# Performance work log

Measured on AMD Instinct MI355X. Metric: run time of the kernel, lower is better.

Reference implementation:

```python
import jax, jax.numpy as jnp
import numpy as np

M, N, P, D = 256, 512, 24, 8


def _se(X, Y):
    # base squared-exponential kernel between point sets: exp(-0.5*||x-y||^2)
    d2 = jnp.sum(X * X, -1)[:, None] + jnp.sum(Y * Y, -1)[None, :] - 2.0 * (X @ Y.T)
    return jnp.exp(-0.5 * jnp.maximum(d2, 0.0))


def _pairwise_dist(X1, A1, X2, A2):
    # vectorized version of the original double loop over metric(f1, f2)
    m, p, d = X1.shape
    n, q, _ = X2.shape
    # cross terms: C[i,j] = a_i @ K(x_i, x_j) @ a_j   (one big Gram, batched quadratic form)
    K12 = _se(X1.reshape(m * p, d), X2.reshape(n * q, d)).reshape(m, p, n, q)
    C = jnp.einsum('iu,iujv,jv->ij', A1, K12, A2)
    # self terms: s_i = a_i @ K(x_i, x_i) @ a_i (computed ONCE, not per inner iteration)
    s1 = jnp.einsum('iu,iuv,iv->i', A1, jax.vmap(_se)(X1, X1), A1)
    s2 = jnp.einsum('ju,juv,jv->j', A2, jax.vmap(_se)(X2, X2), A2)
    d2 = s1[:, None] + s2[None, :] - 2.0 * C
    # matches lax.cond(d2 <= 0, 0.0, sqrt(d2))
    return jnp.sqrt(jnp.maximum(d2, 0.0))


def _kernel(rho, X1, A1, X2, A2):
    # SquaredExponential profile applied to d / sqrt(rho)
    u = _pairwise_dist(X1, A1, X2, A2) / jnp.sqrt(rho)
    return jnp.exp(-0.5 * u * u)


def setup_inputs() -> dict:
    key = jax.random.key(0)
    k = jax.random.split(key, 5)
    return {
        'X_test': jax.random.normal(k[0], (M, P, D), jnp.float32),
        'A_test': 0.2 * jax.random.normal(k[1], (M, P), jnp.float32),
        'X_obs': jax.random.normal(k[2], (N, P, D), jnp.float32),
        'A_obs': 0.2 * jax.random.normal(k[3], (N, P), jnp.float32),
        'observed_ys': jax.random.normal(k[4], (N,), jnp.float32),
        'rho': jnp.asarray(4.0, jnp.float32),
        'g': jnp.asarray(1e-3, jnp.float32),
        'nu': jnp.asarray(1.0, jnp.float32),
        'b': jnp.asarray(0.0, jnp.float32),
    }


def reference(X_test, A_test, X_obs, A_obs, observed_ys, rho, g, nu, b):
    # predict(): Kxx, Kox, Koo then gp_posterior
    Kxx = nu * _kernel(rho, X_test, A_test, X_test, A_test)          # [M, M]
    Kox = nu * _kernel(rho, X_obs, A_obs, X_test, A_test)            # [N, M]
    Koo = nu * (_kernel(rho, X_obs, A_obs, X_obs, A_obs) + g * jnp.eye(N, dtype=X_obs.dtype))

    gain = jnp.linalg.solve(Koo, Kox).T                              # [M, N]
    mean = b + gain @ (observed_ys - b)                              # [M]
    cov = Kxx - gain @ Kox                                           # [M, M]
    Kbx = jnp.ones((1, N), Koo.dtype) @ gain.T                       # [1, M]
    # 1^T Koo^{-1} 1 == inv(Koo).sum(), computed via a solve
    Koo_inv_sum = jnp.linalg.solve(Koo, jnp.ones((N,), Koo.dtype)).sum()
    cov = cov + (1.0 - Kbx).T @ (1.0 - Kbx) / Koo_inv_sum
    # stack mean on top of cov -> [M+1, M]
    return jnp.concatenate([mean[None, :], cov], axis=0)
```

## Files before the change

### kernel.cpp

```cpp
#include <hip/hip_runtime.h>
#include <cmath>

#define M 256
#define N 512
#define P 24
#define D 8

__global__ __launch_bounds__(64) void self_kernel(const float* __restrict__ X_test,
                                                  const float* __restrict__ A_test,
                                                  const float* __restrict__ X_obs,
                                                  const float* __restrict__ A_obs,
                                                  float* __restrict__ s1,
                                                  float* __restrict__ s2,
                                                  float* __restrict__ atT,
                                                  float* __restrict__ atO,
                                                  double* __restrict__ Bc) {
    const int bid = blockIdx.x;
    const int lane = threadIdx.x;
    if (bid == M + N) {
#pragma unroll
        for (int t = 0; t < 8; ++t) Bc[(size_t)256 * 512 + 64 * t + lane] = 1.0;
        return;
    }
    const float* X; const float* A; float* s; float* at; int i;
    if (bid < M) { X = X_test; A = A_test; s = s1; at = atT; i = bid; }
    else         { X = X_obs;  A = A_obs;  s = s2; at = atO; i = bid - M; }
    const float* Xi = X + (size_t)i * P * D;
    const float* Ai = A + (size_t)i * P;
    float acc = 0.f;
#pragma unroll
    for (int t = 0; t < 9; ++t) {
        int idx = lane + 64 * t;
        int u = idx / 24;
        int v = idx - u * 24;
        const float* xu = Xi + u * D;
        const float* xv = Xi + v * D;
        float d2 = 0.f;
#pragma unroll
        for (int d = 0; d < D; ++d) { float df = xu[d] - xv[d]; d2 = fmaf(df, df, d2); }
        acc = fmaf(Ai[u] * Ai[v], __expf(-0.5f * d2), acc);
    }
#pragma unroll
    for (int off = 1; off < 64; off <<= 1) acc += __shfl_xor(acc, off, 64);
    if (lane == 0) s[i] = acc;
    if (lane < 24) {
        const float* xp = Xi + lane * D;
        float q = 0.f;
#pragma unroll
        for (int d = 0; d < D; ++d) q = fmaf(xp[d], xp[d], q);
        at[(size_t)i * P + lane] = Ai[lane] * __expf(-0.5f * q);
    }
}

__global__ __launch_bounds__(128) void gram_kernel(
    const float* __restrict__ Xt, const float* __restrict__ atT, const float* __restrict__ s1,
    const float* __restrict__ Xo, const float* __restrict__ atO, const float* __restrict__ s2,
    const float* __restrict__ rho_p, const float* __restrict__ nu_p, const float* __restrict__ g_p,
    float* __restrict__ KoxT, float* __restrict__ Kxx, double* __restrict__ Koo,
    double* __restrict__ Bc) {
    const int mode = blockIdx.z;
    const int it = blockIdx.x, jt = blockIdx.y;
    const float *X1, *AT1, *S1, *X2, *AT2, *S2;
    if (mode == 0) {
        if (jt > 2 * it + 1) return;
        X1 = Xo; AT1 = atO; S1 = s2; X2 = Xo; AT2 = atO; S2 = s2;
    } else if (mode == 1) {
        if (jt >= 32) return;
        X1 = Xo; AT1 = atO; S1 = s2; X2 = Xt; AT2 = atT; S2 = s1;
    } else {
        if (it >= 16 || jt >= 32 || jt < 2 * it) return;
        X1 = Xt; AT1 = atT; S1 = s1; X2 = Xt; AT2 = atT; S2 = s1;
    }
    const int i0 = it * 16, j0 = jt * 8;
    const int tid = threadIdx.x;
    const int il = tid >> 3, uc = tid & 7;
    const int i = i0 + il;

    __shared__ __align__(16) float X2s[8 * 192];
    __shared__ float A2s[8 * 24];
    __shared__ float S2s[8];
    {
        const float4* gx = (const float4*)(X2 + (size_t)j0 * 192);
        float4* lx = (float4*)X2s;
        for (int idx = tid; idx < 8 * 48; idx += 128) lx[idx] = gx[idx];
        for (int idx = tid; idx < 8 * 24; idx += 128) A2s[idx] = AT2[(size_t)j0 * 24 + idx];
        if (tid < 8) S2s[tid] = S2[j0 + tid];
    }
    __syncthreads();

    float x1r[3][8], at1r[3];
#pragma unroll
    for (int ss = 0; ss < 3; ++ss) {
        const float* p = X1 + ((size_t)i * P + uc * 3 + ss) * D;
#pragma unroll
        for (int d = 0; d < D; ++d) x1r[ss][d] = p[d];
        at1r[ss] = AT1[(size_t)i * P + uc * 3 + ss];
    }
    const float s1i = S1[i];
    const float rho = rho_p[0], nu = nu_p[0], g = g_p[0];

    for (int jj = 0; jj < 8; ++jj) {
        const float* xb = X2s + jj * 192;
        float e0 = 0.f, e1 = 0.f, e2 = 0.f;
#pragma unroll 4
        for (int v = 0; v < 24; ++v) {
            const float4 q0 = ((const float4*)(xb + v * 8))[0];
            const float4 q1 = ((const float4*)(xb + v * 8))[1];
            float x2r[8];
            x2r[0] = q0.x; x2r[1] = q0.y; x2r[2] = q0.z; x2r[3] = q0.w;
            x2r[4] = q1.x; x2r[5] = q1.y; x2r[6] = q1.z; x2r[7] = q1.w;
            const float w2 = A2s[jj * 24 + v];
            float d0 = 0.f, d1 = 0.f, d2 = 0.f;
#pragma unroll
            for (int dd = 0; dd < 8; ++dd) {
                d0 = fmaf(x1r[0][dd], x2r[dd], d0);
                d1 = fmaf(x1r[1][dd], x2r[dd], d1);
                d2 = fmaf(x1r[2][dd], x2r[dd], d2);
            }
            e0 = fmaf(w2, __expf(d0), e0);
            e1 = fmaf(w2, __expf(d1), e1);
            e2 = fmaf(w2, __expf(d2), e2);
        }
        float acc = at1r[0] * e0;
        acc = fmaf(at1r[1], e1, acc);
        acc = fmaf(at1r[2], e2, acc);
        acc += __shfl_xor(acc, 1, 8);
        acc += __shfl_xor(acc, 2, 8);
        acc += __shfl_xor(acc, 4, 8);
        if (uc == 0) {
            const int j = j0 + jj;
            float d2p = fmaxf(s1i + S2s[jj] - 2.f * acc, 0.f);
            float kv = __expf(-0.5f * d2p / rho);
            if (mode == 0) {
                if (j <= i) Koo[(size_t)i * 512 + j] = (double)(nu * (kv + ((i == j) ? g : 0.f)));
            } else if (mode == 1) {
                float val = nu * kv;
                KoxT[(size_t)j * 512 + i] = val;
                Bc[(size_t)j * 512 + i] = (double)val;
            } else {
                float val = nu * kv;
                if (j >= i) {
                    Kxx[(size_t)i * 256 + j] = val;
                    if (j > i) Kxx[(size_t)j * 256 + i] = val;
                }
            }
        }
    }
}

__device__ __forceinline__ double2 ld2t(const double* T, int r, int m) {
    return *(const double2*)(T + r * 64 + 2 * ((m ^ (r >> 2)) & 31));
}
__device__ __forceinline__ void st2t(double* T, int r, int m, double x, double y) {
    double2 v; v.x = x; v.y = y;
    *(double2*)(T + r * 64 + 2 * ((m ^ (r >> 2)) & 31)) = v;
}

__device__ void stage_tile(double* T, const double* G, int ldg, int nrows) {
    const int tid = threadIdx.x;
#pragma unroll
    for (int e = 0; e < 8; ++e) {
        int idx = tid + 256 * e, r = idx >> 5, m = idx & 31;
        double x = 0.0, y = 0.0;
        if (r < nrows) {
            double2 v = *(const double2*)(G + (size_t)r * ldg + 2 * m);
            x = v.x; y = v.y;
        }
        st2t(T, r, m, x, y);
    }
}
__device__ void stage_tile_f(double* T, const float* G, int ldg) {
    const int tid = threadIdx.x;
#pragma unroll
    for (int e = 0; e < 8; ++e) {
        int idx = tid + 256 * e, r = idx >> 5, m = idx & 31;
        float2 v = *(const float2*)(G + (size_t)r * ldg + 2 * m);
        st2t(T, r, m, (double)v.x, (double)v.y);
    }
}

__device__ __forceinline__ void mac4x4(const double* At, const double* Bt,
                                       double acc[4][4], int tx, int ty) {
#pragma unroll 4
    for (int m = 0; m < 32; ++m) {
        double2 a[4], b[4];
#pragma unroll
        for (int j = 0; j < 4; ++j) a[j] = ld2t(At, 4 * ty + j, m);
#pragma unroll
        for (int j = 0; j < 4; ++j) b[j] = ld2t(Bt, 4 * tx + j, m);
#pragma unroll
        for (int r = 0; r < 4; ++r)
#pragma unroll
            for (int c = 0; c < 4; ++c)
                acc[r][c] = fma(a[r].y, b[c].y, fma(a[r].x, b[c].x, acc[r][c]));
    }
}

__device__ void stt_tile(double* T, const double v[4][4], int tx, int ty) {
#pragma unroll
    for (int r = 0; r < 4; ++r)
#pragma unroll
        for (int mp = 0; mp < 2; ++mp)
            st2t(T, 4 * ty + r, 2 * tx + mp, v[r][2 * mp], v[r][2 * mp + 1]);
}

#define LO(i, j) ((i) * ((i) + 1) / 2 + (j))

__device__ void factor64(double (*sA)[65], double (*sX)[65], double* sW,
                         double* Wp, double* WTp, int p) {
    const int tid = threadIdx.x;
    {
        double* f = &sX[0][0];
        for (int idx = tid; idx < 64 * 65; idx += 256) f[idx] = 0.0;
    }
    __syncthreads();
    for (int q = 0; q < 4; ++q) {
        const int b0 = 16 * q;
        if (tid < 64) {
            const int rr = tid >> 2, gg = tid & 3;
            double a[4], x[4];
#pragma unroll
            for (int j = 0; j < 4; ++j) {
                int cc = 4 * gg + j;
                a[j] = (cc <= rr) ? sA[b0 + rr][b0 + cc] : sA[b0 + cc][b0 + rr];
                x[j] = 0.0;
            }
#pragma unroll
            for (int k = 0; k < 16; ++k) {
                double akk = __shfl(a[k & 3], (k << 2) | (k >> 2), 64);
                double rd = 1.0 / sqrt(akk);
                if (gg == (k >> 2) && rr >= k)
                    a[k & 3] = (rr == k) ? akk * rd : a[k & 3] * rd;
                if (k < 15) {
                    double lrk = __shfl(a[k & 3], (rr << 2) | (k >> 2), 64);
                    double lck[4];
#pragma unroll
                    for (int j = 0; j < 4; ++j)
                        lck[j] = __shfl(a[k & 3], ((4 * gg + j) << 2) | (k >> 2), 64);
#pragma unroll
                    for (int j = 0; j < 4; ++j) {
                        int cc = 4 * gg + j;
                        if (rr > k && cc > k) a[j] = fma(-lrk, lck[j], a[j]);
                    }
                }
            }
#pragma unroll
            for (int r2 = 0; r2 < 16; ++r2) {
                double s0 = 0.0, s1 = 0.0, s2 = 0.0, s3 = 0.0;
#pragma unroll
                for (int t = 0; t < r2; ++t) {
                    double lrt = __shfl(a[t & 3], (r2 << 2) | (t >> 2), 64);
                    s0 = fma(lrt, __shfl(x[0], (t << 2) | gg, 64), s0);
                    s1 = fma(lrt, __shfl(x[1], (t << 2) | gg, 64), s1);
                    s2 = fma(lrt, __shfl(x[2], (t << 2) | gg, 64), s2);
                    s3 = fma(lrt, __shfl(x[3], (t << 2) | gg, 64), s3);
                }
                double lrr = __shfl(a[r2 & 3], (r2 << 2) | (r2 >> 2), 64);
                double rdr = 1.0 / lrr;
                if (rr == r2) {
                    double sv[4] = {s0, s1, s2, s3};
#pragma unroll
                    for (int j = 0; j < 4; ++j) {
                        int cc = 4 * gg + j;
                        x[j] = (cc <= r2) ? (((cc == r2) ? 1.0 : 0.0) - sv[j]) * rdr : 0.0;
                    }
                }
            }
#pragma unroll
            for (int j = 0; j < 4; ++j) {
                int cc = 4 * gg + j;
                if (cc <= rr) sA[b0 + rr][b0 + cc] = a[j];
                sX[b0 + rr][b0 + cc] = x[j];
            }
        }
        __syncthreads();
        if (q < 3) {
            const int nrows = 48 - b0;
            const int cells = nrows * 16;
            double tv[3];
#pragma unroll
            for (int ii = 0; ii < 3; ++ii) {
                int idx = tid + 256 * ii;
                tv[ii] = 0.0;
                if (idx < cells) {
                    int a2 = b0 + 16 + (idx >> 4), cc = idx & 15;
                    double acc = 0.0;
                    for (int t = 0; t <= cc; ++t)
                        acc = fma(sA[a2][b0 + t], sX[b0 + cc][b0 + t], acc);
                    tv[ii] = acc;
                }
            }
            __syncthreads();
#pragma unroll
            for (int ii = 0; ii < 3; ++ii) {
                int idx = tid + 256 * ii;
                if (idx < cells) {
                    int a2 = b0 + 16 + (idx >> 4), cc = idx & 15;
                    sA[a2][b0 + cc] = tv[ii];
                }
            }
            __syncthreads();
            for (int idx = tid; idx < nrows * nrows; idx += 256) {
                int r = b0 + 16 + idx / nrows, cc = b0 + 16 + idx % nrows;
                if (cc <= r) {
                    double acc = 0.0;
#pragma unroll
                    for (int t = 0; t < 16; ++t)
                        acc = fma(sA[r][b0 + t], sA[cc][b0 + t], acc);
                    sA[r][cc] -= acc;
                }
            }
            __syncthreads();
        }
    }
    for (int d = 1; d <= 3; ++d) {
        __syncthreads();
        int npairs = 4 - d;
        for (int i2 = tid; i2 < npairs * 256; i2 += 256) {
            int pr = i2 >> 8, cell = i2 & 255, r = cell >> 4, c = cell & 15;
            int qc = pr, qr = pr + d;
            double w = 0.0;
            for (int t = 16 * qc; t < 16 * qr; ++t)
                w = fma(sA[16 * qr + r][t], sX[t][16 * qc + c], w);
            sW[pr * 272 + r * 17 + c] = w;
        }
        __syncthreads();
        for (int i2 = tid; i2 < npairs * 256; i2 += 256) {
            int pr = i2 >> 8, cell = i2 & 255, r = cell >> 4, c = cell & 15;
            int qc = pr, qr = pr + d;
            double x2 = 0.0;
            for (int t = 0; t <= r; ++t)
                x2 = fma(sX[16 * qr + r][16 * qr + t], sW[pr * 272 + t * 17 + c], x2);
            sX[16 * qr + r][16 * qc + c] = -x2;
        }
    }
    __syncthreads();
    {
        const size_t off = (size_t)LO(p, p) * 4096;
        for (int idx = tid; idx < 4096; idx += 256) {
            int r = idx >> 6, c = idx & 63;
            double xv = sX[r][c];
            Wp[off + idx] = xv;
            WTp[off + (size_t)c * 64 + r] = xv;
        }
    }
    __syncthreads();
}

__global__ __launch_bounds__(256) void factor0_kernel(const double* __restrict__ A,
                                                      double* __restrict__ Wp,
                                                      double* __restrict__ WTp) {
    __shared__ double smem[9136];
    double (*fA)[65] = (double(*)[65])smem;
    double (*fX)[65] = (double(*)[65])(smem + 4160);
    double* fW = smem + 8320;
    const int tid = threadIdx.x;
    for (int idx = tid; idx < 4096; idx += 256) {
        int r = idx >> 6, c = idx & 63;
        fA[r][c] = (c <= r) ? A[(size_t)r * 512 + c] : 0.0;
    }
    __syncthreads();
    factor64(fA, fX, fW, Wp, WTp, 0);
}

__device__ void upd_tile(double* smem, double* A, double* LL,
                         double* Wp, double* WTp, int p, int s, int tx, int ty) {
    double* T0 = smem;
    double* T1 = smem + 4096;
    double* T2 = smem + 8192;
    int bi = 0;
    while (s >= bi + 1) { s -= bi + 1; ++bi; }
    const int bj = s;
    const int I = p + 1 + bi, J = p + 1 + bj;
    const bool diag = (I == J);

    stage_tile(T0, A + (size_t)I * 64 * 512 + p * 64, 512, 64);
    if (!diag) stage_tile(T1, A + (size_t)J * 64 * 512 + p * 64, 512, 64);
    stage_tile(T2, Wp + (size_t)LO(p, p) * 4096, 64, 64);
    __syncthreads();

    double lip[4][4] = {}, ljp[4][4] = {};
    mac4x4(T0, T2, lip, tx, ty);
    if (!diag) mac4x4(T1, T2, ljp, tx, ty);
    __syncthreads();
    stt_tile(T0, lip, tx, ty);
    if (!diag) stt_tile(T1, ljp, tx, ty);
    if (diag) {
#pragma unroll
        for (int r = 0; r < 4; ++r)
#pragma unroll
            for (int c = 0; c < 4; ++c)
                LL[(size_t)(I * 64 + 4 * ty + r) * 512 + p * 64 + 4 * tx + c] = lip[r][c];
    }
    __syncthreads();

    double acc[4][4] = {};
    mac4x4(T0, diag ? T0 : T1, acc, tx, ty);

    double* Aij = A + (size_t)I * 64 * 512 + (size_t)J * 64;
    if (bi == 0 && bj == 0) {
        __syncthreads();
        double (*fA)[65] = (double(*)[65])smem;
        double (*fX)[65] = (double(*)[65])(smem + 4160);
        double* fW = smem + 8320;
#pragma unroll
        for (int r = 0; r < 4; ++r)
#pragma unroll
            for (int c = 0; c < 4; ++c) {
                int rr = 4 * ty + r, cc = 4 * tx + c;
                fA[rr][cc] = (cc <= rr) ? (Aij[(size_t)rr * 512 + cc] - acc[r][c]) : 0.0;
            }
        __syncthreads();
        factor64(fA, fX, fW, Wp, WTp, p + 1);
    } else {
#pragma unroll
        for (int r = 0; r < 4; ++r)
#pragma unroll
            for (int c = 0; c < 4; ++c) {
                int rr = 4 * ty + r, cc = 4 * tx + c;
                if (!diag || cc <= rr)
                    Aij[(size_t)rr * 512 + cc] -= acc[r][c];
            }
    }
}

__device__ void wrow_tile(double* smem, const double* LL,
                          double* Wp, double* WTp, int p, int J, int tx, int ty) {
    double* T0 = smem;
    double* T1 = smem + 4096;
    double* T2 = smem + 8192;
    stage_tile(T2, Wp + (size_t)LO(p, p) * 4096, 64, 64);
    double S[4][4] = {};
    for (int K = J; K < p; ++K) {
        stage_tile(T0, LL + (size_t)(p * 64) * 512 + K * 64, 512, 64);
        stage_tile(T1, WTp + (size_t)LO(K, J) * 4096, 64, 64);
        __syncthreads();
        mac4x4(T0, T1, S, tx, ty);
        __syncthreads();
    }
#pragma unroll
    for (int c = 0; c < 4; ++c)
#pragma unroll
        for (int rp = 0; rp < 2; ++rp)
            st2t(T0, 4 * tx + c, 2 * ty + rp, S[2 * rp][c], S[2 * rp + 1][c]);
    __syncthreads();
    double X[4][4] = {};
    mac4x4(T2, T0, X, tx, ty);
    const size_t wo = (size_t)LO(p, J) * 4096;
#pragma unroll
    for (int r = 0; r < 4; ++r)
#pragma unroll
        for (int c = 0; c < 4; ++c) {
            Wp[wo + (size_t)(4 * ty + r) * 64 + 4 * tx + c] = -X[r][c];
            WTp[wo + (size_t)(4 * tx + c) * 64 + 4 * ty + r] = -X[r][c];
        }
}

__global__ __launch_bounds__(256) void upd_kernel(double* __restrict__ A,
                                                  double* __restrict__ LL,
                                                  double* __restrict__ Wp,
                                                  double* __restrict__ WTp,
                                                  int p) {
    __shared__ double smem[12288];
    const int tx = threadIdx.x & 15, ty = threadIdx.x >> 4;
    const int nupd = (7 - p) * (8 - p) / 2;
    if ((int)blockIdx.x < nupd)
        upd_tile(smem, A, LL, Wp, WTp, p, blockIdx.x, tx, ty);
    else
        wrow_tile(smem, LL, Wp, WTp, p, blockIdx.x - nupd, tx, ty);
}

__global__ __launch_bounds__(256) void wrow7_kernel(const double* __restrict__ LL,
                                                    double* __restrict__ Wp,
                                                    double* __restrict__ WTp) {
    __shared__ double smem[12288];
    const int tx = threadIdx.x & 15, ty = threadIdx.x >> 4;
    wrow_tile(smem, LL, Wp, WTp, 7, blockIdx.x, tx, ty);
}

__global__ __launch_bounds__(256) void gemm1_kernel(const double* __restrict__ Wp,
                                                    const double* __restrict__ Bc,
                                                    double* __restrict__ Tbuf) {
    __shared__ double smem[8192];
    const int blk = blockIdx.x;
    const int i = blk / 5, ct = blk % 5, c0 = ct * 64;
    const int nr = (257 - c0 < 64) ? (257 - c0) : 64;
    double* T0 = smem;
    double* T1 = smem + 4096;
    const int tx = threadIdx.x & 15, ty = threadIdx.x >> 4;
    double acc[4][4] = {};
    for (int j = 0; j <= i; ++j) {
        stage_tile(T0, Wp + (size_t)LO(i, j) * 4096, 64, 64);
        stage_tile(T1, Bc + (size_t)c0 * 512 + j * 64, 512, nr);
        __syncthreads();
        mac4x4(T0, T1, acc, tx, ty);
        __syncthreads();
    }
#pragma unroll
    for (int r = 0; r < 4; ++r)
#pragma unroll
        for (int c = 0; c < 4; ++c) {
            int cc = c0 + 4 * tx + c;
            if (cc < 257) Tbuf[(size_t)cc * 512 + i * 64 + 4 * ty + r] = acc[r][c];
        }
}

__global__ __launch_bounds__(256) void gemm2_kernel(const double* __restrict__ WTp,
                                                    const double* __restrict__ Tbuf,
                                                    double* __restrict__ Bc) {
    __shared__ double smem[8192];
    const int blk = blockIdx.x;
    const int i = blk / 5, ct = blk % 5, c0 = ct * 64;
    const int nr = (257 - c0 < 64) ? (257 - c0) : 64;
    double* T0 = smem;
    double* T1 = smem + 4096;
    const int tx = threadIdx.x & 15, ty = threadIdx.x >> 4;
    double acc[4][4] = {};
    for (int j = i; j < 8; ++j) {
        stage_tile(T0, WTp + (size_t)LO(j, i) * 4096, 64, 64);
        stage_tile(T1, Tbuf + (size_t)c0 * 512 + j * 64, 512, nr);
        __syncthreads();
        mac4x4(T0, T1, acc, tx, ty);
        __syncthreads();
    }
#pragma unroll
    for (int r = 0; r < 4; ++r)
#pragma unroll
        for (int c = 0; c < 4; ++c) {
            int cc = c0 + 4 * tx + c;
            if (cc < 257) Bc[(size_t)cc * 512 + i * 64 + 4 * ty + r] = acc[r][c];
        }
}

__global__ __launch_bounds__(256) void colreduce_kernel(const double* __restrict__ Z,
                                                        const float* __restrict__ ys,
                                                        const float* __restrict__ b_p,
                                                        float* __restrict__ out,
                                                        double* __restrict__ kbx,
                                                        double* __restrict__ Sp) {
    const int lane = threadIdx.x & 63, w = threadIdx.x >> 6;
    const int c = blockIdx.x * 4 + w;
    if (c >= 257) return;
    const double b = (double)b_p[0];
    double s0 = 0.0, s1 = 0.0;
#pragma unroll
    for (int t = 0; t < 8; ++t) {
        int n = lane + 64 * t;
        double zv = Z[(size_t)c * 512 + n];
        s0 += zv;
        s1 = fma(zv, (double)ys[n] - b, s1);
    }
#pragma unroll
    for (int off = 1; off < 64; off <<= 1) {
        s0 += __shfl_xor(s0, off, 64);
        s1 += __shfl_xor(s1, off, 64);
    }
    if (lane == 0) {
        if (c < 256) { out[c] = (float)(b + s1); kbx[c] = s0; }
        else Sp[0] = s0;
    }
}

__global__ __launch_bounds__(256) void cov_kernel(const double* __restrict__ Z,
                                                  const float* __restrict__ KoxT,
                                                  const float* __restrict__ Kxx,
                                                  const double* __restrict__ kbx,
                                                  const double* __restrict__ Sp,
                                                  float* __restrict__ out) {
    __shared__ double smem[8192];
    const int bi = blockIdx.x >> 2, bj = blockIdx.x & 3;
    double* T0 = smem;
    double* T1 = smem + 4096;
    const int tx = threadIdx.x & 15, ty = threadIdx.x >> 4;
    double acc[4][4] = {};
    for (int kt = 0; kt < 8; ++kt) {
        stage_tile(T0, Z + (size_t)(bi * 64) * 512 + kt * 64, 512, 64);
        stage_tile_f(T1, KoxT + (size_t)(bj * 64) * 512 + kt * 64, 512);
        __syncthreads();
        mac4x4(T0, T1, acc, tx, ty);
        __syncthreads();
    }
    const double S = Sp[0];
#pragma unroll
    for (int r = 0; r < 4; ++r) {
        int i = bi * 64 + 4 * ty + r;
        double ki = 1.0 - kbx[i];
#pragma unroll
        for (int c = 0; c < 4; ++c) {
            int j = bj * 64 + 4 * tx + c;
            double corr = ki * (1.0 - kbx[j]) / S;
            out[(size_t)(1 + i) * 256 + j] =
                (float)((double)Kxx[(size_t)i * 256 + j] - acc[r][c] + corr);
        }
    }
}

extern "C" void kernel_launch(void* const* d_in, const int* in_sizes, int n_in,
                              void* d_out, int out_size, void* d_ws, size_t ws_size,
                              hipStream_t stream) {
    const float* X_test = (const float*)d_in[0];
    const float* A_test = (const float*)d_in[1];
    const float* X_obs  = (const float*)d_in[2];
    const float* A_obs  = (const float*)d_in[3];
    const float* ys     = (const float*)d_in[4];
    const float* rho_p  = (const float*)d_in[5];
    const float* g_p    = (const float*)d_in[6];
    const float* nu_p   = (const float*)d_in[7];
    const float* b_p    = (const float*)d_in[8];
    float* out = (float*)d_out;
    char* ws = (char*)d_ws;

    double* Koo  = (double*)(ws + 0);
    double* LL   = (double*)(ws + 2097152);
    double* Bc   = (double*)(ws + 4194304);
    float*  KoxT = (float*) (ws + 5246976);
    float*  Kxx  = (float*) (ws + 5771264);
    float*  s1v  = (float*) (ws + 6033408);
    float*  s2v  = (float*) (ws + 6034432);
    double* kbx  = (double*)(ws + 6036480);
    double* Sp   = (double*)(ws + 6038528);
    double* Wp   = (double*)(ws + 6039552);
    double* WTp  = (double*)(ws + 7219200);
    double* Tbuf = Koo;
    float*  atT  = (float*)(ws + 2097152);
    float*  atO  = (float*)(ws + 2097152 + 24576);

    self_kernel<<<M + N + 1, 64, 0, stream>>>(X_test, A_test, X_obs, A_obs,
                                              s1v, s2v, atT, atO, Bc);

    gram_kernel<<<dim3(32, 64, 3), 128, 0, stream>>>(X_test, atT, s1v,
                                                     X_obs, atO, s2v,
                                                     rho_p, nu_p, g_p,
                                                     KoxT, Kxx, Koo, Bc);

    factor0_kernel<<<1, 256, 0, stream>>>(Koo, Wp, WTp);
    for (int p = 0; p < 7; ++p) {
        int nb = (7 - p) * (8 - p) / 2 + p;
        upd_kernel<<<nb, 256, 0, stream>>>(Koo, LL, Wp, WTp, p);
    }
    wrow7_kernel<<<7, 256, 0, stream>>>(LL, Wp, WTp);

    gemm1_kernel<<<40, 256, 0, stream>>>(Wp, Bc, Tbuf);
    gemm2_kernel<<<40, 256, 0, stream>>>(WTp, Tbuf, Bc);
    colreduce_kernel<<<65, 256, 0, stream>>>(Bc, ys, b_p, out, kbx, Sp);
    cov_kernel<<<16, 256, 0, stream>>>(Bc, KoxT, Kxx, kbx, Sp, out);
}
```

Baseline: 975.3 us.

## Replace blocked 64x64 Cholesky+inverse with single-wavefront register-resident LDL factorization

The blocked 16x16 Cholesky and triangular-inverse routine, which ran on 256 threads with many barriers, is replaced by a single 64-lane wavefront. Each lane holds one matrix row in 64 registers and performs an LDL-style elimination, then forward substitution to build the inverse factor. Hardware v_rcp_f64 and v_rsq_f64 with Newton refinement replace the division and sqrt, and the per-step barriers go away. In exchange, only 64 threads do the work while the rest of the block idles, register pressure is very high (spill risk), and the serial 64-step loop is longer.

```diff
diff --git a/kernel.cpp b/kernel.cpp
--- a/kernel.cpp
+++ b/kernel.cpp
@@ -206,161 +206,89 @@
 
 #define LO(i, j) ((i) * ((i) + 1) / 2 + (j))
 
-__device__ void factor64(double (*sA)[65], double (*sX)[65], double* sW,
-                         double* Wp, double* WTp, int p) {
-    const int tid = threadIdx.x;
-    {
-        double* f = &sX[0][0];
-        for (int idx = tid; idx < 64 * 65; idx += 256) f[idx] = 0.0;
-    }
-    __syncthreads();
-    for (int q = 0; q < 4; ++q) {
-        const int b0 = 16 * q;
-        if (tid < 64) {
-            const int rr = tid >> 2, gg = tid & 3;
-            double a[4], x[4];
-#pragma unroll
-            for (int j = 0; j < 4; ++j) {
-                int cc = 4 * gg + j;
-                a[j] = (cc <= rr) ? sA[b0 + rr][b0 + cc] : sA[b0 + cc][b0 + rr];
-                x[j] = 0.0;
-            }
-#pragma unroll
-            for (int k = 0; k < 16; ++k) {
-                double akk = __shfl(a[k & 3], (k << 2) | (k >> 2), 64);
-                double rd = 1.0 / sqrt(akk);
-                if (gg == (k >> 2) && rr >= k)
-                    a[k & 3] = (rr == k) ? akk * rd : a[k & 3] * rd;
-                if (k < 15) {
-                    double lrk = __shfl(a[k & 3], (rr << 2) | (k >> 2), 64);
-                    double lck[4];
-#pragma unroll
-                    for (int j = 0; j < 4; ++j)
-                        lck[j] = __shfl(a[k & 3], ((4 * gg + j) << 2) | (k >> 2), 64);
-#pragma unroll
-                    for (int j = 0; j < 4; ++j) {
-                        int cc = 4 * gg + j;
-                        if (rr > k && cc > k) a[j] = fma(-lrk, lck[j], a[j]);
-                    }
-                }
-            }
-#pragma unroll
-            for (int r2 = 0; r2 < 16; ++r2) {
-                double s0 = 0.0, s1 = 0.0, s2 = 0.0, s3 = 0.0;
-#pragma unroll
-                for (int t = 0; t < r2; ++t) {
-                    double lrt = __shfl(a[t & 3], (r2 << 2) | (t >> 2), 64);
-                    s0 = fma(lrt, __shfl(x[0], (t << 2) | gg, 64), s0);
-                    s1 = fma(lrt, __shfl(x[1], (t << 2) | gg, 64), s1);
-                    s2 = fma(lrt, __shfl(x[2], (t << 2) | gg, 64), s2);
-                    s3 = fma(lrt, __shfl(x[3], (t << 2) | gg, 64), s3);
-                }
-                double lrr = __shfl(a[r2 & 3], (r2 << 2) | (r2 >> 2), 64);
-                double rdr = 1.0 / lrr;
-                if (rr == r2) {
-                    double sv[4] = {s0, s1, s2, s3};
-#pragma unroll
-                    for (int j = 0; j < 4; ++j) {
-                        int cc = 4 * gg + j;
-                        x[j] = (cc <= r2) ? (((cc == r2) ? 1.0 : 0.0) - sv[j]) * rdr : 0.0;
-                    }
-                }
-            }
-#pragma unroll
-            for (int j = 0; j < 4; ++j) {
-                int cc = 4 * gg + j;
-                if (cc <= rr) sA[b0 + rr][b0 + cc] = a[j];
-                sX[b0 + rr][b0 + cc] = x[j];
-            }
-        }
-        __syncthreads();
-        if (q < 3) {
-            const int nrows = 48 - b0;
-            const int cells = nrows * 16;
-            double tv[3];
-#pragma unroll
-            for (int ii = 0; ii < 3; ++ii) {
-                int idx = tid + 256 * ii;
-                tv[ii] = 0.0;
-                if (idx < cells) {
-                    int a2 = b0 + 16 + (idx >> 4), cc = idx & 15;
-                    double acc = 0.0;
-                    for (int t = 0; t <= cc; ++t)
-                        acc = fma(sA[a2][b0 + t], sX[b0 + cc][b0 + t], acc);
-                    tv[ii] = acc;
-                }
-            }
-            __syncthreads();
-#pragma unroll
-            for (int ii = 0; ii < 3; ++ii) {
-                int idx = tid + 256 * ii;
-                if (idx < cells) {
-                    int a2 = b0 + 16 + (idx >> 4), cc = idx & 15;
-                    sA[a2][b0 + cc] = tv[ii];
-                }
-            }
-            __syncthreads();
-            for (int idx = tid; idx < nrows * nrows; idx += 256) {
-                int r = b0 + 16 + idx / nrows, cc = b0 + 16 + idx % nrows;
-                if (cc <= r) {
-                    double acc = 0.0;
-#pragma unroll
-                    for (int t = 0; t < 16; ++t)
-                        acc = fma(sA[r][b0 + t], sA[cc][b0 + t], acc);
-                    sA[r][cc] -= acc;
-                }
-            }
-            __syncthreads();
-        }
-    }
-    for (int d = 1; d <= 3; ++d) {
-        __syncthreads();
-        int npairs = 4 - d;
-        for (int i2 = tid; i2 < npairs * 256; i2 += 256) {
-            int pr = i2 >> 8, cell = i2 & 255, r = cell >> 4, c = cell & 15;
-            int qc = pr, qr = pr + d;
-            double w = 0.0;
-            for (int t = 16 * qc; t < 16 * qr; ++t)
-                w = fma(sA[16 * qr + r][t], sX[t][16 * qc + c], w);
-            sW[pr * 272 + r * 17 + c] = w;
-        }
-        __syncthreads();
-        for (int i2 = tid; i2 < npairs * 256; i2 += 256) {
-            int pr = i2 >> 8, cell = i2 & 255, r = cell >> 4, c = cell & 15;
-            int qc = pr, qr = pr + d;
-            double x2 = 0.0;
-            for (int t = 0; t <= r; ++t)
-                x2 = fma(sX[16 * qr + r][16 * qr + t], sW[pr * 272 + t * 17 + c], x2);
-            sX[16 * qr + r][16 * qc + c] = -x2;
-        }
-    }
-    __syncthreads();
-    {
-        const size_t off = (size_t)LO(p, p) * 4096;
-        for (int idx = tid; idx < 4096; idx += 256) {
-            int r = idx >> 6, c = idx & 63;
-            double xv = sX[r][c];
-            Wp[off + idx] = xv;
-            WTp[off + (size_t)c * 64 + r] = xv;
-        }
-    }
-    __syncthreads();
+__device__ __forceinline__ double frcp(double d) {
+    double r;
+    asm("v_rcp_f64 %0, %1" : "=v"(r) : "v"(d));
+    double e = fma(-d, r, 1.0); r = fma(r, e, r);
+    e = fma(-d, r, 1.0); r = fma(r, e, r);
+    return r;
+}
+__device__ __forceinline__ double frsq(double d) {
+    double r;
+    asm("v_rsq_f64 %0, %1" : "=v"(r) : "v"(d));
+    double t = -0.5 * d * r; r = r * fma(t, r, 1.5);
+    t = -0.5 * d * r; r = r * fma(t, r, 1.5);
+    return r;
+}
+
+__device__ void factor64v3(double* sA, double* colbuf,
+                           double* __restrict__ Wp, double* __restrict__ WTp,
+                           int p) {
+    const int lane = threadIdx.x;
+    double a[64];
+#pragma unroll
+    for (int c = 0; c < 64; ++c) {
+        int ad = (c <= lane) ? (lane * 65 + c) : (c * 65 + lane);
+        a[c] = sA[ad];
+    }
+    double myinv = 0.0, myd = 1.0;
+#pragma unroll
+    for (int k = 0; k < 64; ++k) {
+        colbuf[lane] = a[k];
+        double dk = colbuf[k];
+        double inv = frcp(dk);
+        if (lane == k) { myinv = inv; myd = dk; }
+        double s = (lane > k) ? a[k] * inv : 0.0;
+#pragma unroll
+        for (int c = k + 1; c < 64; ++c)
+            a[c] = fma(-s, colbuf[c], a[c]);
+    }
+    const double myrs = frsq(myd);
+    colbuf[lane] = myinv;
+#pragma unroll
+    for (int c = 0; c < 64; ++c) a[c] *= colbuf[c];
+#pragma unroll
+    for (int c = 0; c < 64; ++c) sA[lane * 65 + c] = a[c];
+#pragma unroll
+    for (int r = 0; r < 64; ++r) a[r] = (lane == r) ? 1.0 : 0.0;
+#pragma unroll
+    for (int r = 1; r < 64; ++r) {
+        const double* Lr = sA + r * 65;
+        double a0 = 0.0, a1 = 0.0, a2 = 0.0, a3 = 0.0;
+#pragma unroll
+        for (int t = 0; t < r; ++t) {
+            double lv = Lr[t];
+            if ((t & 3) == 0) a0 = fma(lv, a[t], a0);
+            else if ((t & 3) == 1) a1 = fma(lv, a[t], a1);
+            else if ((t & 3) == 2) a2 = fma(lv, a[t], a2);
+            else a3 = fma(lv, a[t], a3);
+        }
+        a[r] -= (a0 + a1) + (a2 + a3);
+    }
+    colbuf[lane] = myrs;
+#pragma unroll
+    for (int r = 0; r < 64; ++r) a[r] *= colbuf[r];
+    const size_t off = (size_t)LO(p, p) * 4096;
+#pragma unroll
+    for (int r = 0; r < 64; ++r) Wp[off + (size_t)r * 64 + lane] = a[r];
+#pragma unroll
+    for (int r = 0; r < 64; r += 2) {
+        double2 v; v.x = a[r]; v.y = a[r + 1];
+        *(double2*)(WTp + off + (size_t)lane * 64 + r) = v;
+    }
 }
 
 __global__ __launch_bounds__(256) void factor0_kernel(const double* __restrict__ A,
                                                       double* __restrict__ Wp,
                                                       double* __restrict__ WTp) {
-    __shared__ double smem[9136];
-    double (*fA)[65] = (double(*)[65])smem;
-    double (*fX)[65] = (double(*)[65])(smem + 4160);
-    double* fW = smem + 8320;
+    __shared__ double smem[4160 + 64];
     const int tid = threadIdx.x;
     for (int idx = tid; idx < 4096; idx += 256) {
         int r = idx >> 6, c = idx & 63;
-        fA[r][c] = (c <= r) ? A[(size_t)r * 512 + c] : 0.0;
+        if (c <= r) smem[r * 65 + c] = A[(size_t)r * 512 + c];
     }
     __syncthreads();
-    factor64(fA, fX, fW, Wp, WTp, 0);
+    if (tid < 64) factor64v3(smem, smem + 4160, Wp, WTp, 0);
 }
 
 __device__ void upd_tile(double* smem, double* A, double* LL,
@@ -400,18 +328,15 @@
     double* Aij = A + (size_t)I * 64 * 512 + (size_t)J * 64;
     if (bi == 0 && bj == 0) {
         __syncthreads();
-        double (*fA)[65] = (double(*)[65])smem;
-        double (*fX)[65] = (double(*)[65])(smem + 4160);
-        double* fW = smem + 8320;
 #pragma unroll
         for (int r = 0; r < 4; ++r)
 #pragma unroll
             for (int c = 0; c < 4; ++c) {
                 int rr = 4 * ty + r, cc = 4 * tx + c;
-                fA[rr][cc] = (cc <= rr) ? (Aij[(size_t)rr * 512 + cc] - acc[r][c]) : 0.0;
+                if (cc <= rr) smem[rr * 65 + cc] = Aij[(size_t)rr * 512 + cc] - acc[r][c];
             }
         __syncthreads();
-        factor64(fA, fX, fW, Wp, WTp, p + 1);
+        if (threadIdx.x < 64) factor64v3(smem, smem + 4160, Wp, WTp, p + 1);
     } else {
 #pragma unroll
         for (int r = 0; r < 4; ++r)
```

Measured after the change: 902.9 us. 7.4% less time.
